# Performance work log

Measured on AMD Instinct MI355X. Metric: run time of the kernel, lower is better.

The kernel has to match this reference:

```python
import jax, jax.numpy as jnp
import numpy as np

B, S, D = 2, 2048, 1024
H, HKV = 16, 4
HD = D // H          # 64
NREP = H // HKV      # 4
EPS = 1e-6
ROPE_BASE = 10000.0


def setup_inputs() -> dict:
    key = jax.random.key(0)
    ks = jax.random.split(key, 6)
    std = 0.02
    return {
        "x": jax.random.normal(ks[0], (B, S, D), dtype=jnp.float32),
        "Wq": jax.random.normal(ks[1], (D, H * HD), dtype=jnp.float32) * std,
        "Wk": jax.random.normal(ks[2], (D, HKV * HD), dtype=jnp.float32) * std,
        "Wv": jax.random.normal(ks[3], (D, HKV * HD), dtype=jnp.float32) * std,
        "Wo": jax.random.normal(ks[4], (D, D), dtype=jnp.float32) * std,
        "norm_w": jnp.ones((D,), dtype=jnp.float32),
    }


def _rope_cos_sin(seq_len, head_dim, dtype):
    inv_freq = 1.0 / (ROPE_BASE ** (jnp.arange(0, head_dim, 2, dtype=jnp.float32) / head_dim))
    t = jnp.arange(seq_len, dtype=jnp.float32)
    freqs = jnp.outer(t, inv_freq)                 # [S, HD/2]
    emb = jnp.concatenate([freqs, freqs], axis=-1)  # [S, HD]
    return jnp.cos(emb).astype(dtype), jnp.sin(emb).astype(dtype)


def _rotate_half(x):
    x1, x2 = jnp.split(x, 2, axis=-1)
    return jnp.concatenate([-x2, x1], axis=-1)


def _apply_rope(x, cos, sin):
    # x: [B, nh, S, HD]; cos/sin: [S, HD]
    return x * cos[None, None] + _rotate_half(x) * sin[None, None]


def reference(x, Wq, Wk, Wv, Wo, norm_w):
    b, s, _ = x.shape
    q = (x @ Wq).reshape(b, s, H, HD).transpose(0, 2, 1, 3)      # [B,H,S,HD]
    k = (x @ Wk).reshape(b, s, HKV, HD).transpose(0, 2, 1, 3)    # [B,HKV,S,HD]
    v = (x @ Wv).reshape(b, s, HKV, HD).transpose(0, 2, 1, 3)

    cos, sin = _rope_cos_sin(s, HD, x.dtype)
    q = _apply_rope(q, cos, sin)
    k = _apply_rope(k, cos, sin)

    # repeat kv heads to match q heads
    k = jnp.repeat(k, NREP, axis=1)   # [B,H,S,HD]
    v = jnp.repeat(v, NREP, axis=1)

    scale = HD ** -0.5
    scores = jnp.einsum('bhqd,bhkd->bhqk', q, k) * scale   # [B,H,S,S]
    attn = jax.nn.softmax(scores, axis=-1)
    out = jnp.einsum('bhqk,bhkd->bhqd', attn, v)            # [B,H,S,HD]
    out = out.transpose(0, 2, 1, 3).reshape(b, s, D)
    out = out @ Wo

    # RMSNorm
    rms = jnp.sqrt(jnp.mean(out * out, axis=-1, keepdims=True) + EPS)
    out = out / rms * norm_w
    return out
```

## Files before the change

### kernel.cpp

```cpp
#include <hip/hip_runtime.h>
#include <hip/hip_bf16.h>
#include <stdint.h>
#include <math.h>

typedef __bf16 bf16x8 __attribute__((ext_vector_type(8)));
typedef float f32x4 __attribute__((ext_vector_type(4)));
typedef float f32x16 __attribute__((ext_vector_type(16)));

#define B_    2
#define S_    2048
#define D_    1024
#define H_    16
#define HKV_  4
#define HD_   64
#define MTOT  4096
#define NQKV  1536
#define BHS   65536

#define ZERO16 {0.f,0.f,0.f,0.f,0.f,0.f,0.f,0.f,0.f,0.f,0.f,0.f,0.f,0.f,0.f,0.f}

__device__ __forceinline__ unsigned short f2bf(float f) {
  union { float f; unsigned u; } v; v.f = f;
  unsigned r = (v.u + 0x7FFFu + ((v.u >> 16) & 1u)) >> 16;
  return (unsigned short)r;
}

__device__ __forceinline__ float bf2f(unsigned short u) {
  union { unsigned u; float f; } v; v.u = (unsigned)u << 16; return v.f;
}

__device__ __forceinline__ float fast_exp2(float x) {
  return __builtin_amdgcn_exp2f(x);
}

__device__ __forceinline__ unsigned cvt_pk_bf16(float lo, float hi) {
  unsigned r;
  asm("v_cvt_pk_bf16_f32 %0, %1, %2" : "=v"(r) : "v"(lo), "v"(hi));
  return r;
}

__device__ __forceinline__ void gl_lds16(const void* g, void* l) {
  __builtin_amdgcn_global_load_lds((const __attribute__((address_space(1))) void*)g,
                                   (__attribute__((address_space(3))) void*)l, 16, 0, 0);
}

__global__ __launch_bounds__(256) void k_pre(const float* __restrict__ Wq, const float* __restrict__ Wk,
                                             const float* __restrict__ Wv, const float* __restrict__ Wo,
                                             const float* __restrict__ x,
                                             unsigned short* __restrict__ wqkvt,
                                             unsigned short* __restrict__ wot,
                                             unsigned short* __restrict__ xb,
                                             float* __restrict__ cost, float* __restrict__ sint) {
  int bid = blockIdx.x, tid = threadIdx.x;
  if (bid < 640) {
    const float* src; unsigned short* dst; int ldsrc, cb, rb;
    if (bid < 256)      { src = Wq; dst = wqkvt;                          ldsrc = 1024; cb = (bid & 15) * 64; rb = (bid >> 4) * 64; }
    else if (bid < 320) { int i = bid - 256; src = Wk; dst = wqkvt + (size_t)1024 * 1024; ldsrc = 256; cb = (i & 3) * 64; rb = (i >> 2) * 64; }
    else if (bid < 384) { int i = bid - 320; src = Wv; dst = wqkvt + (size_t)1280 * 1024; ldsrc = 256; cb = (i & 3) * 64; rb = (i >> 2) * 64; }
    else                { int i = bid - 384; src = Wo; dst = wot;         ldsrc = 1024; cb = (i & 15) * 64; rb = (i >> 4) * 64; }
    __shared__ unsigned short T[64][72];
    for (int rep = 0; rep < 4; ++rep) {
      int idx = rep * 256 + tid;
      int r = idx >> 4, seg = idx & 15;
      float4 v = *(const float4*)&src[(size_t)(rb + r) * ldsrc + cb + seg * 4];
      T[seg*4+0][r] = f2bf(v.x);
      T[seg*4+1][r] = f2bf(v.y);
      T[seg*4+2][r] = f2bf(v.z);
      T[seg*4+3][r] = f2bf(v.w);
    }
    __syncthreads();
    for (int rep = 0; rep < 2; ++rep) {
      int idx = rep * 256 + tid;
      int c = idx >> 3, seg = idx & 7;
      *(uint4*)&dst[(size_t)(cb + c) * 1024 + rb + seg * 8] = *(const uint4*)&T[c][seg * 8];
    }
  } else if (bid < 896) {
    int idx = (bid - 640) * 256 + tid;
    int s = idx >> 5, i = idx & 31;
    double inv = exp(-(double)i / 32.0 * log(10000.0));
    double ang = (double)s * inv;
    cost[idx] = (float)cos(ang);
    sint[idx] = (float)sin(ang);
  } else {
    int i = (bid - 896) * 256 + tid;
    const int n4 = MTOT * D_ / 4;
    for (; i < n4; i += 1024 * 256) {
      float4 v = ((const float4*)x)[i];
      ushort4 o;
      o.x = f2bf(v.x); o.y = f2bf(v.y); o.z = f2bf(v.z); o.w = f2bf(v.w);
      ((ushort4*)xb)[i] = o;
    }
  }
}

__global__ __launch_bounds__(256) void k_gemm_qkv(const unsigned short* __restrict__ A,
                                                  const unsigned short* __restrict__ Bt,
                                                  const float* __restrict__ cost,
                                                  const float* __restrict__ sint,
                                                  unsigned short* __restrict__ Qb,
                                                  unsigned short* __restrict__ Kb,
                                                  unsigned short* __restrict__ Vt) {
  int nb = blockIdx.x, mb = blockIdx.y;
  __shared__ unsigned short Arena[2][12288];
  int tid = threadIdx.x, lane = tid & 63, w = tid >> 6;
  int wr = w >> 1, wc = w & 1;
  f32x4 acc[2][4];
  for (int m = 0; m < 2; ++m) for (int n = 0; n < 4; ++n) acc[m][n] = (f32x4){0.f, 0.f, 0.f, 0.f};

  const int rl = lane >> 3;
  const int csw = ((lane & 7) ^ rl) * 8;

  auto stage = [&](int buf, int kt) {
    for (int j = 0; j < 2; ++j)
      gl_lds16(&A[(size_t)(mb * 64 + w * 16 + j * 8 + rl) * D_ + kt * 64 + csw],
               &Arena[buf][(w * 16 + j * 8) * 64]);
    for (int j = 0; j < 4; ++j)
      gl_lds16(&Bt[(size_t)(nb * 128 + w * 32 + j * 8 + rl) * D_ + kt * 64 + csw],
               &Arena[buf][4096 + (w * 32 + j * 8) * 64]);
  };
  stage(0, 0);
  const int NT = D_ / 64;
  int cur = 0;
  const int lr = lane & 15, lg = lane >> 4, swl = lane & 7;
  for (int kt = 0; kt < NT; ++kt) {
    __syncthreads();
    if (kt + 1 < NT) stage(cur ^ 1, kt + 1);
    #pragma unroll
    for (int kk = 0; kk < 2; ++kk) {
      int ch = ((kk * 4 + lg) ^ swl) * 8;
      bf16x8 af[2], bfr[4];
      for (int m = 0; m < 2; ++m) af[m]  = *(const bf16x8*)&Arena[cur][(wr * 32 + m * 16 + lr) * 64 + ch];
      for (int n = 0; n < 4; ++n) bfr[n] = *(const bf16x8*)&Arena[cur][4096 + (wc * 64 + n * 16 + lr) * 64 + ch];
      for (int m = 0; m < 2; ++m)
        for (int n = 0; n < 4; ++n)
          acc[m][n] = __builtin_amdgcn_mfma_f32_16x16x32_bf16(af[m], bfr[n], acc[m][n], 0, 0, 0);
    }
    cur ^= 1;
  }

  const int lq = (lane >> 4) * 4;
  const int b = mb >> 5;
  const int s0 = (mb & 31) * 64;

  if (nb < 10) {
    const float QSCALE = 0.18033688011112042f;
    float scl = (nb < 8) ? QSCALE : 1.f;
    #pragma unroll
    for (int m = 0; m < 2; ++m) {
      #pragma unroll
      for (int n = 0; n < 4; ++n) {
        int gc = nb * 128 + wc * 64 + n * 16 + lr;
        int d  = gc & 63, d2 = d & 31;
        float sgn = (d < 32) ? -1.f : 1.f;
        unsigned short* dst;
        if (nb < 8) {
          int h = gc >> 6;
          dst = Qb + (((size_t)(b * H_ + h)) * S_) * HD_ + d;
        } else {
          int hk = (gc - 1024) >> 6;
          dst = Kb + (((size_t)(b * HKV_ + hk)) * S_) * HD_ + d;
        }
        #pragma unroll
        for (int r = 0; r < 4; ++r) {
          int s = s0 + wr * 32 + m * 16 + lq + r;
          float c  = cost[s * 32 + d2];
          float sn = sint[s * 32 + d2];
          float xv = acc[m][n][r];
          float xp = acc[m][n ^ 2][r];
          float o = (xv * c + sgn * xp * sn) * scl;
          dst[(size_t)s * HD_] = f2bf(o);
        }
      }
    }
  } else {
    __syncthreads();
    unsigned short* T = &Arena[0][0];
    #pragma unroll
    for (int m = 0; m < 2; ++m)
      #pragma unroll
      for (int n = 0; n < 4; ++n)
        #pragma unroll
        for (int r = 0; r < 4; ++r) {
          int c = wc * 64 + n * 16 + lr;
          int rw = wr * 32 + m * 16 + lq + r;
          T[c * 72 + rw] = f2bf(acc[m][n][r]);
        }
    __syncthreads();
    {
      int j = tid >> 1, q = tid & 1;
      int v_off = (nb - 10) * 128 + j;
      int hk = v_off >> 6, dl = v_off & 63;
      unsigned short* dst = Vt + (((size_t)(b * HKV_ + hk)) * HD_ + dl) * S_ + s0 + q * 32;
      const unsigned short* srcp = &T[j * 72 + q * 32];
      #pragma unroll
      for (int k2 = 0; k2 < 4; ++k2)
        *(uint4*)&dst[k2 * 8] = *(const uint4*)&srcp[k2 * 8];
    }
  }
}

__global__ __launch_bounds__(256) void k_gemm_bt(const unsigned short* __restrict__ A,
                                                 const unsigned short* __restrict__ Bt,
                                                 unsigned short* __restrict__ C0,
                                                 unsigned short* __restrict__ C1,
                                                 int M, int N, int Kfull) {
  int nb = blockIdx.x, mb = blockIdx.y, z = blockIdx.z;
  int kbase = z * (Kfull >> 1);
  int Klen = Kfull >> 1;
  unsigned short* C = z ? C1 : C0;
  __shared__ unsigned short Arena[2][12288];
  int tid = threadIdx.x, lane = tid & 63, w = tid >> 6;
  int wr = w >> 1, wc = w & 1;
  f32x4 acc[2][4];
  for (int m = 0; m < 2; ++m) for (int n = 0; n < 4; ++n) acc[m][n] = (f32x4){0.f, 0.f, 0.f, 0.f};

  const int rl = lane >> 3;
  const int csw = ((lane & 7) ^ rl) * 8;

  auto stage = [&](int buf, int kt) {
    for (int j = 0; j < 2; ++j)
      gl_lds16(&A[(size_t)(mb * 64 + w * 16 + j * 8 + rl) * Kfull + kbase + kt * 64 + csw],
               &Arena[buf][(w * 16 + j * 8) * 64]);
    for (int j = 0; j < 4; ++j)
      gl_lds16(&Bt[(size_t)(nb * 128 + w * 32 + j * 8 + rl) * Kfull + kbase + kt * 64 + csw],
               &Arena[buf][4096 + (w * 32 + j * 8) * 64]);
  };
  stage(0, 0);
  int NT = Klen / 64;
  int cur = 0;
  const int lr = lane & 15, lg = lane >> 4, swl = lane & 7;
  for (int kt = 0; kt < NT; ++kt) {
    __syncthreads();
    if (kt + 1 < NT) stage(cur ^ 1, kt + 1);
    #pragma unroll
    for (int kk = 0; kk < 2; ++kk) {
      int ch = ((kk * 4 + lg) ^ swl) * 8;
      bf16x8 af[2], bfr[4];
      for (int m = 0; m < 2; ++m) af[m]  = *(const bf16x8*)&Arena[cur][(wr * 32 + m * 16 + lr) * 64 + ch];
      for (int n = 0; n < 4; ++n) bfr[n] = *(const bf16x8*)&Arena[cur][4096 + (wc * 64 + n * 16 + lr) * 64 + ch];
      for (int m = 0; m < 2; ++m)
        for (int n = 0; n < 4; ++n)
          acc[m][n] = __builtin_amdgcn_mfma_f32_16x16x32_bf16(af[m], bfr[n], acc[m][n], 0, 0, 0);
    }
    cur ^= 1;
  }
  int lq = (lane >> 4) * 4;
  for (int m = 0; m < 2; ++m)
    for (int n = 0; n < 4; ++n)
      for (int r = 0; r < 4; ++r)
        C[(size_t)(mb * 64 + wr * 32 + m * 16 + lq + r) * N + nb * 128 + wc * 64 + n * 16 + lr] =
            f2bf(acc[m][n][r]);
}

__global__ __launch_bounds__(512, 2) void k_attn(const unsigned short* __restrict__ Q,
                                                 const unsigned short* __restrict__ K,
                                                 const unsigned short* __restrict__ Vt,
                                                 unsigned short* __restrict__ Ob) {
  int wg = ((blockIdx.x & 7) << 6) | (blockIdx.x >> 3);
  int qt = wg & 15;
  int bh = wg >> 4;
  int b = bh >> 4, h = bh & 15, hk = h >> 2;
  const unsigned short* Qp = Q + (((size_t)(b * H_ + h)) * S_ + qt * 128) * HD_;
  const unsigned short* Kp = K + ((size_t)(b * HKV_ + hk)) * S_ * HD_;
  const unsigned short* Vp = Vt + ((size_t)(b * HKV_ + hk)) * HD_ * S_;

  __shared__ unsigned short Lds[2 * 16384];

  const int tid = threadIdx.x, lane = tid & 63, w = tid >> 6;
  const int g  = w >> 2;
  const int wl = w & 3;
  const int col = lane & 31;
  const int hi  = lane >> 5;
  const int sw  = lane & 7;
  const int kv0 = g * (S_ / 2);
  const int gbase = g * 16384;

  const unsigned short* pka[4];
  #pragma unroll
  for (int kc = 0; kc < 4; ++kc)
    pka[kc] = &Lds[gbase + col * 64 + ((kc * 2 + hi) ^ sw) * 8];

  bf16x8 qf[4];
  {
    const unsigned short* qrow = Qp + (size_t)(wl * 32 + col) * HD_;
    #pragma unroll
    for (int dc = 0; dc < 4; ++dc)
      qf[dc] = *(const bf16x8*)&qrow[dc * 16 + hi * 8];
  }

  f32x16 oacc0 = ZERO16, oacc1 = ZERO16;
  float l_run = 0.f;

  const int rl = lane >> 3, cs = lane & 7;
  const int row0 = wl * 16 + rl;
  const int csrc = (cs ^ (row0 & 7)) * 8;
  const unsigned short* srcK = &Kp[(size_t)(kv0 + row0) * HD_ + csrc];
  const unsigned short* srcV = &Vp[(size_t)row0 * S_ + kv0 + csrc];

  auto stage = [&](int be) {
    gl_lds16(srcK,           &Lds[gbase + be + (wl * 16) * 64]);
    gl_lds16(srcK + 8 * HD_, &Lds[gbase + be + (wl * 16 + 8) * 64]);
    gl_lds16(srcV,           &Lds[gbase + be + 8192 + (wl * 16) * 64]);
    gl_lds16(srcV + 8 * S_,  &Lds[gbase + be + 8192 + (wl * 16 + 8) * 64]);
    srcK += 64 * HD_;
    srcV += 64;
  };

  auto compute = [&](int be) {
    bf16x8 pf[4];
    float ps0 = 0.f, ps1 = 0.f, ps2 = 0.f, ps3 = 0.f;
    #pragma unroll
    for (int blk2 = 0; blk2 < 2; ++blk2) {
      f32x16 st = ZERO16;
      __builtin_amdgcn_s_setprio(1);
      #pragma unroll
      for (int kc = 0; kc < 4; ++kc) {
        bf16x8 kf = *(const bf16x8*)(pka[kc] + be + blk2 * 2048);
        st = __builtin_amdgcn_mfma_f32_32x32x16_bf16(kf, qf[kc], st, 0, 0, 0);
      }
      __builtin_amdgcn_s_setprio(0);
      #pragma unroll
      for (int i = 0; i < 16; i += 4) {
        st[i]     = fast_exp2(st[i]);
        st[i + 1] = fast_exp2(st[i + 1]);
        st[i + 2] = fast_exp2(st[i + 2]);
        st[i + 3] = fast_exp2(st[i + 3]);
        ps0 += st[i]; ps1 += st[i + 1]; ps2 += st[i + 2]; ps3 += st[i + 3];
      }
      #pragma unroll
      for (int kcl = 0; kcl < 2; ++kcl) {
        int base = kcl * 8;
        unsigned u0 = cvt_pk_bf16(st[base + 0], st[base + 1]);
        unsigned u1 = cvt_pk_bf16(st[base + 2], st[base + 3]);
        unsigned u2 = cvt_pk_bf16(st[base + 4], st[base + 5]);
        unsigned u3 = cvt_pk_bf16(st[base + 6], st[base + 7]);
        asm("v_permlane32_swap_b32 %0, %1" : "+v"(u0), "+v"(u2));
        asm("v_permlane32_swap_b32 %0, %1" : "+v"(u1), "+v"(u3));
        union { unsigned u[4]; bf16x8 v; } pk;
        pk.u[0] = u0; pk.u[1] = u1; pk.u[2] = u2; pk.u[3] = u3;
        pf[blk2 * 2 + kcl] = pk.v;
      }
    }
    float psum = (ps0 + ps1) + (ps2 + ps3);
    psum += __shfl_xor(psum, 32);
    l_run += psum;
    __builtin_amdgcn_s_setprio(1);
    #pragma unroll
    for (int kc = 0; kc < 4; ++kc) {
      bf16x8 v0 = *(const bf16x8*)(pka[kc] + be + 8192);
      bf16x8 v1 = *(const bf16x8*)(pka[kc] + be + 8192 + 2048);
      oacc0 = __builtin_amdgcn_mfma_f32_32x32x16_bf16(v0, pf[kc], oacc0, 0, 0, 0);
      oacc1 = __builtin_amdgcn_mfma_f32_32x32x16_bf16(v1, pf[kc], oacc1, 0, 0, 0);
    }
    __builtin_amdgcn_s_setprio(0);
  };

  stage(0);
  for (int it = 0; it < 8; ++it) {
    __syncthreads();
    stage(4096);
    compute(0);
    __syncthreads();
    if (it < 7) stage(0);
    compute(4096);
  }

  __syncthreads();
  float* xch = (float*)Lds;
  if (g == 0) {
    float* slot = xch + ((size_t)wl * 64 + lane) * 33;
    #pragma unroll
    for (int i = 0; i < 16; ++i) { slot[i] = oacc0[i]; slot[16 + i] = oacc1[i]; }
    slot[32] = l_run;
  }
  __syncthreads();
  if (g == 1) {
    const float* slot = xch + ((size_t)wl * 64 + lane) * 33;
    float rinv = 1.f / (l_run + slot[32]);
    int qrow = qt * 128 + wl * 32 + col;
    unsigned short* ob = Ob + ((size_t)(b * S_ + qrow)) * D_ + h * 64;
    #pragma unroll
    for (int rr = 0; rr < 4; ++rr) {
      ushort4 o0, o1;
      o0.x = f2bf((oacc0[rr*4+0] + slot[rr*4+0]) * rinv);
      o0.y = f2bf((oacc0[rr*4+1] + slot[rr*4+1]) * rinv);
      o0.z = f2bf((oacc0[rr*4+2] + slot[rr*4+2]) * rinv);
      o0.w = f2bf((oacc0[rr*4+3] + slot[rr*4+3]) * rinv);
      o1.x = f2bf((oacc1[rr*4+0] + slot[16+rr*4+0]) * rinv);
      o1.y = f2bf((oacc1[rr*4+1] + slot[16+rr*4+1]) * rinv);
      o1.z = f2bf((oacc1[rr*4+2] + slot[16+rr*4+2]) * rinv);
      o1.w = f2bf((oacc1[rr*4+3] + slot[16+rr*4+3]) * rinv);
      *(ushort4*)&ob[8 * rr + 4 * hi]      = o0;
      *(ushort4*)&ob[32 + 8 * rr + 4 * hi] = o1;
    }
  }
}

__global__ __launch_bounds__(256) void k_rmsnorm(const unsigned short* __restrict__ in0,
                                                 const unsigned short* __restrict__ in1,
                                                 const float* __restrict__ wt,
                                                 float* __restrict__ out) {
  int row = blockIdx.x, tid = threadIdx.x;
  ushort4 u0 = *(const ushort4*)&in0[(size_t)row * D_ + tid * 4];
  ushort4 u1 = *(const ushort4*)&in1[(size_t)row * D_ + tid * 4];
  float x0 = bf2f(u0.x) + bf2f(u1.x);
  float x1 = bf2f(u0.y) + bf2f(u1.y);
  float x2 = bf2f(u0.z) + bf2f(u1.z);
  float x3 = bf2f(u0.w) + bf2f(u1.w);
  float ss = x0 * x0 + x1 * x1 + x2 * x2 + x3 * x3;
  for (int o = 32; o >= 1; o >>= 1) ss += __shfl_xor(ss, o);
  __shared__ float red[4];
  if ((tid & 63) == 0) red[tid >> 6] = ss;
  __syncthreads();
  float tot = red[0] + red[1] + red[2] + red[3];
  float rinv = 1.f / sqrtf(tot * (1.f / 1024.f) + 1e-6f);
  float4 wv = ((const float4*)wt)[tid];
  float4 o;
  o.x = x0 * rinv * wv.x;
  o.y = x1 * rinv * wv.y;
  o.z = x2 * rinv * wv.z;
  o.w = x3 * rinv * wv.w;
  ((float4*)(out + (size_t)row * D_))[tid] = o;
}

extern "C" void kernel_launch(void* const* d_in, const int* in_sizes, int n_in,
                              void* d_out, int out_size, void* d_ws, size_t ws_size,
                              hipStream_t stream) {
  const float* x  = (const float*)d_in[0];
  const float* Wq = (const float*)d_in[1];
  const float* Wk = (const float*)d_in[2];
  const float* Wv = (const float*)d_in[3];
  const float* Wo = (const float*)d_in[4];
  const float* nw = (const float*)d_in[5];
  float* out = (float*)d_out;

  char* p = (char*)d_ws;
  unsigned short* xb    = (unsigned short*)p; p += (size_t)MTOT * D_ * 2;
  char*           slot  = p;                  p += (size_t)18 * 1024 * 1024;
  unsigned short* wqkvt = (unsigned short*)p; p += (size_t)NQKV * D_ * 2;
  unsigned short* wot   = (unsigned short*)p; p += (size_t)D_ * D_ * 2;
  unsigned short* qb    = (unsigned short*)p; p += (size_t)B_ * H_ * S_ * HD_ * 2;
  unsigned short* kb    = (unsigned short*)p; p += (size_t)B_ * HKV_ * S_ * HD_ * 2;
  unsigned short* vtb   = (unsigned short*)p; p += (size_t)B_ * HKV_ * HD_ * S_ * 2;
  char*           big2  = p;                  p += (size_t)MTOT * D_ * 2 * 2;
  float*          mlold = (float*)p;          p += (size_t)2 * BHS * 4;
  float*          cost  = (float*)p;          p += (size_t)S_ * 32 * 4;
  float*          sint  = (float*)p;          p += (size_t)S_ * 32 * 4;
  (void)mlold;

  unsigned short* attnb   = (unsigned short*)big2;
  unsigned short* proj_p0 = (unsigned short*)slot;
  unsigned short* proj_p1 = (unsigned short*)(slot + (size_t)MTOT * D_ * 2);

  k_pre<<<1920, 256, 0, stream>>>(Wq, Wk, Wv, Wo, x, wqkvt, wot, xb, cost, sint);

  k_gemm_qkv<<<dim3(NQKV / 128, MTOT / 64), 256, 0, stream>>>(xb, wqkvt, cost, sint, qb, kb, vtb);
  k_attn<<<512, 512, 0, stream>>>(qb, kb, vtb, attnb);
  k_gemm_bt<<<dim3(D_ / 128, MTOT / 64, 2), 256, 0, stream>>>(attnb, wot, proj_p0, proj_p1, MTOT, D_, D_);
  k_rmsnorm<<<MTOT, 256, 0, stream>>>(proj_p0, proj_p1, nw, out);
}
```

Measured before the change: 94.12 us.

## Single-buffer attention KV tiles in LDS and exchange partials as bf16

The attention kernel's LDS allocation is halved: the K/V double buffer becomes a single buffer, with stage, sync, compute and sync run serially for each tile. The cross-group output exchange is packed as bf16 pairs so it fits in the smaller LDS footprint. The aim is to fit more workgroups per CU by cutting LDS use. In exchange, global-to-LDS loads no longer overlap compute, and the partial accumulator from one group is rounded to bf16 before the sum.

New measurement: 95.14 us. No clear change (+1.1%).

```diff
diff --git a/kernel.cpp b/kernel.cpp
--- a/kernel.cpp
+++ b/kernel.cpp
@@ -264,7 +264,7 @@
   const unsigned short* Kp = K + ((size_t)(b * HKV_ + hk)) * S_ * HD_;
   const unsigned short* Vp = Vt + ((size_t)(b * HKV_ + hk)) * HD_ * S_;
 
-  __shared__ unsigned short Lds[2 * 16384];
+  __shared__ unsigned short Lds[2 * 8192];
 
   const int tid = threadIdx.x, lane = tid & 63, w = tid >> 6;
   const int g  = w >> 2;
@@ -273,7 +273,7 @@
   const int hi  = lane >> 5;
   const int sw  = lane & 7;
   const int kv0 = g * (S_ / 2);
-  const int gbase = g * 16384;
+  const int gbase = g * 8192;
 
   const unsigned short* pka[4];
   #pragma unroll
@@ -297,16 +297,16 @@
   const unsigned short* srcK = &Kp[(size_t)(kv0 + row0) * HD_ + csrc];
   const unsigned short* srcV = &Vp[(size_t)row0 * S_ + kv0 + csrc];
 
-  auto stage = [&](int be) {
-    gl_lds16(srcK,           &Lds[gbase + be + (wl * 16) * 64]);
-    gl_lds16(srcK + 8 * HD_, &Lds[gbase + be + (wl * 16 + 8) * 64]);
-    gl_lds16(srcV,           &Lds[gbase + be + 8192 + (wl * 16) * 64]);
-    gl_lds16(srcV + 8 * S_,  &Lds[gbase + be + 8192 + (wl * 16 + 8) * 64]);
+  auto stage = [&]() {
+    gl_lds16(srcK,           &Lds[gbase + (wl * 16) * 64]);
+    gl_lds16(srcK + 8 * HD_, &Lds[gbase + (wl * 16 + 8) * 64]);
+    gl_lds16(srcV,           &Lds[gbase + 4096 + (wl * 16) * 64]);
+    gl_lds16(srcV + 8 * S_,  &Lds[gbase + 4096 + (wl * 16 + 8) * 64]);
     srcK += 64 * HD_;
     srcV += 64;
   };
 
-  auto compute = [&](int be) {
+  auto compute = [&]() {
     bf16x8 pf[4];
     float ps0 = 0.f, ps1 = 0.f, ps2 = 0.f, ps3 = 0.f;
     #pragma unroll
@@ -315,7 +315,7 @@
       __builtin_amdgcn_s_setprio(1);
       #pragma unroll
       for (int kc = 0; kc < 4; ++kc) {
-        bf16x8 kf = *(const bf16x8*)(pka[kc] + be + blk2 * 2048);
+        bf16x8 kf = *(const bf16x8*)(pka[kc] + blk2 * 2048);
         st = __builtin_amdgcn_mfma_f32_32x32x16_bf16(kf, qf[kc], st, 0, 0, 0);
       }
       __builtin_amdgcn_s_setprio(0);
@@ -347,49 +347,51 @@
     __builtin_amdgcn_s_setprio(1);
     #pragma unroll
     for (int kc = 0; kc < 4; ++kc) {
-      bf16x8 v0 = *(const bf16x8*)(pka[kc] + be + 8192);
-      bf16x8 v1 = *(const bf16x8*)(pka[kc] + be + 8192 + 2048);
+      bf16x8 v0 = *(const bf16x8*)(pka[kc] + 4096);
+      bf16x8 v1 = *(const bf16x8*)(pka[kc] + 4096 + 2048);
       oacc0 = __builtin_amdgcn_mfma_f32_32x32x16_bf16(v0, pf[kc], oacc0, 0, 0, 0);
       oacc1 = __builtin_amdgcn_mfma_f32_32x32x16_bf16(v1, pf[kc], oacc1, 0, 0, 0);
     }
     __builtin_amdgcn_s_setprio(0);
   };
 
-  stage(0);
-  for (int it = 0; it < 8; ++it) {
-    __syncthreads();
-    stage(4096);
-    compute(0);
-    __syncthreads();
-    if (it < 7) stage(0);
-    compute(4096);
-  }
-
-  __syncthreads();
-  float* xch = (float*)Lds;
+  for (int t = 0; t < 16; ++t) {
+    stage();
+    __syncthreads();
+    compute();
+    __syncthreads();
+  }
+
+  unsigned* xch = (unsigned*)Lds;
   if (g == 0) {
-    float* slot = xch + ((size_t)wl * 64 + lane) * 33;
-    #pragma unroll
-    for (int i = 0; i < 16; ++i) { slot[i] = oacc0[i]; slot[16 + i] = oacc1[i]; }
-    slot[32] = l_run;
+    unsigned* slot = xch + ((size_t)wl * 64 + lane) * 17;
+    #pragma unroll
+    for (int i = 0; i < 8; ++i) slot[i]     = cvt_pk_bf16(oacc0[2*i], oacc0[2*i+1]);
+    #pragma unroll
+    for (int i = 0; i < 8; ++i) slot[8 + i] = cvt_pk_bf16(oacc1[2*i], oacc1[2*i+1]);
+    union { float f; unsigned u; } lu; lu.f = l_run;
+    slot[16] = lu.u;
   }
   __syncthreads();
   if (g == 1) {
-    const float* slot = xch + ((size_t)wl * 64 + lane) * 33;
-    float rinv = 1.f / (l_run + slot[32]);
+    const unsigned* slot = xch + ((size_t)wl * 64 + lane) * 17;
+    union { float f; unsigned u; } lu; lu.u = slot[16];
+    float rinv = 1.f / (l_run + lu.f);
     int qrow = qt * 128 + wl * 32 + col;
     unsigned short* ob = Ob + ((size_t)(b * S_ + qrow)) * D_ + h * 64;
     #pragma unroll
     for (int rr = 0; rr < 4; ++rr) {
       ushort4 o0, o1;
-      o0.x = f2bf((oacc0[rr*4+0] + slot[rr*4+0]) * rinv);
-      o0.y = f2bf((oacc0[rr*4+1] + slot[rr*4+1]) * rinv);
-      o0.z = f2bf((oacc0[rr*4+2] + slot[rr*4+2]) * rinv);
-      o0.w = f2bf((oacc0[rr*4+3] + slot[rr*4+3]) * rinv);
-      o1.x = f2bf((oacc1[rr*4+0] + slot[16+rr*4+0]) * rinv);
-      o1.y = f2bf((oacc1[rr*4+1] + slot[16+rr*4+1]) * rinv);
-      o1.z = f2bf((oacc1[rr*4+2] + slot[16+rr*4+2]) * rinv);
-      o1.w = f2bf((oacc1[rr*4+3] + slot[16+rr*4+3]) * rinv);
+      unsigned pa0 = slot[rr * 2], pa1 = slot[rr * 2 + 1];
+      unsigned pb0 = slot[8 + rr * 2], pb1 = slot[8 + rr * 2 + 1];
+      o0.x = f2bf((oacc0[rr*4+0] + bf2f((unsigned short)(pa0 & 0xFFFF)))  * rinv);
+      o0.y = f2bf((oacc0[rr*4+1] + bf2f((unsigned short)(pa0 >> 16)))     * rinv);
+      o0.z = f2bf((oacc0[rr*4+2] + bf2f((unsigned short)(pa1 & 0xFFFF)))  * rinv);
+      o0.w = f2bf((oacc0[rr*4+3] + bf2f((unsigned short)(pa1 >> 16)))     * rinv);
+      o1.x = f2bf((oacc1[rr*4+0] + bf2f((unsigned short)(pb0 & 0xFFFF)))  * rinv);
+      o1.y = f2bf((oacc1[rr*4+1] + bf2f((unsigned short)(pb0 >> 16)))     * rinv);
+      o1.z = f2bf((oacc1[rr*4+2] + bf2f((unsigned short)(pb1 & 0xFFFF)))  * rinv);
+      o1.w = f2bf((oacc1[rr*4+3] + bf2f((unsigned short)(pb1 >> 16)))     * rinv);
       *(ushort4*)&ob[8 * rr + 4 * hi]      = o0;
       *(ushort4*)&ob[32 + 8 * rr + 4 * hi] = o1;
     }
```
